# Kernel optimization log

Measured on AMD Instinct MI355X. Metric: run time of the kernel, lower is better.

The kernel has to match this reference:

```python
import jax, jax.numpy as jnp
import numpy as np

# --- static config (matches init_kwargs) ---
B, T, D, L = 32, 1024, 256, 10          # batch, signal length (2^L), feature dim, wavelet levels
V = T * D                                # |V| = 262144 graph nodes
ETA = 0.1
STEPS = 2                                # reaction_steps
INV_SQRT2 = 0.7071067811865476
BAND_SIZES = [T >> L] + [T >> l for l in range(L, 0, -1)]  # approx + details coarse->fine (n_levels+1 bands)


def haar_dwt(x):
    """x: (B,T,D) -> coeffs (B,T,D), layout [approx_L, d_L, d_{L-1}, ..., d_1]."""
    a = x
    details = []
    for _ in range(L):
        e, o = a[:, 0::2], a[:, 1::2]
        details.append((e - o) * INV_SQRT2)
        a = (e + o) * INV_SQRT2
    return jnp.concatenate([a] + details[::-1], axis=1)


def haar_idwt(c):
    """c: (B,T,D) in [approx, coarse..fine detail] layout -> signal (B,T,D)."""
    a = c[:, : T >> L]
    pos = T >> L
    for l in range(L, 0, -1):
        n = T >> l
        d = c[:, pos : pos + n]
        pos += n
        e = (a + d) * INV_SQRT2
        o = (a - d) * INV_SQRT2
        a = jnp.stack([e, o], axis=2).reshape(c.shape[0], 2 * n, D)  # interleave even/odd
    return a


def wavelet_linear(sig, W, b):
    """Per-band Linear(D->D): band i of the time axis uses W[i], b[i]."""
    outs = []
    pos = 0
    for i, n in enumerate(BAND_SIZES):
        seg = sig[:, pos : pos + n]  # (B, n, D)
        pos += n
        outs.append(jnp.einsum('btd,de->bte', seg, W[i]) + b[i])
    return jnp.concatenate(outs, axis=1)


def setup_inputs() -> dict:
    key = jax.random.key(0)
    k1, k2, k3, k4 = jax.random.split(key, 4)
    rho = jax.random.normal(k1, (B, V), dtype=jnp.float32)
    node_w = 0.5 + jax.random.uniform(k2, (V,), dtype=jnp.float32)            # graph node scaling (invertible)
    W = jax.random.normal(k3, (L + 1, D, D), dtype=jnp.float32) * 0.05        # per-band predictor weights
    b = jax.random.normal(k4, (L + 1, D), dtype=jnp.float32) * 0.01           # per-band bias
    return {"rho": rho, "node_w": node_w, "W": W, "b": b}


def reference(rho, node_w, W, b):
    for _ in range(STEPS):
        coeffs = (rho * node_w).reshape(B, T, D)          # graph.rho_to_coeffs
        coeffs_signal = haar_idwt(coeffs)                 # haar_idwt_1d
        predicted_signal = wavelet_linear(coeffs_signal, W, b)  # WaveletLinear predictor
        predicted_coeffs = haar_dwt(predicted_signal)     # haar_dwt_1d
        predicted_rho = predicted_coeffs.reshape(B, V) / node_w  # graph.coeffs_to_rho
        rho = rho - ETA * (rho - predicted_rho)           # PC error-reduction step
    return rho
```

## Files before the change

kernel.cpp:

```cpp
#include <hip/hip_runtime.h>
#include <hip/hip_bf16.h>

#define NB 32
#define NT 1024
#define ND 256
#define SP 264
#define ETA 0.1f
#define INVS 0.70710678118654752440f

typedef short bf16x8 __attribute__((ext_vector_type(8)));
typedef float f32x4  __attribute__((ext_vector_type(4)));

__device__ inline unsigned short f2bf(float f){
  __hip_bfloat16 h = __float2bfloat16(f);
  return *reinterpret_cast<unsigned short*>(&h);
}
__device__ inline float bf2f(unsigned short u){
  return __uint_as_float(((unsigned int)u) << 16);
}

template<int N>
__device__ inline void idwtT(float* a, const float* d){
#pragma unroll
  for (int i = N-1; i >= 0; --i){
    float av = a[i], dv = d[i];
    a[2*i]   = (av + dv) * INVS;
    a[2*i+1] = (av - dv) * INVS;
  }
}
template<int N>
__device__ inline void dwtT(float* a, float* d){
#pragma unroll
  for (int i = 0; i < N; ++i){
    float e = a[2*i], o = a[2*i+1];
    a[i] = (e + o) * INVS;
    d[i] = (e - o) * INVS;
  }
}
template<int N>
__device__ inline void dwt_sel2(float* x, int pj, float& pdet,
                                int j0, float& y0, int j1, float& y1){
#pragma unroll
  for (int i = 0; i < N; ++i){
    float e = x[2*i], o = x[2*i+1];
    float aa = (e + o) * INVS, dd = (e - o) * INVS;
    x[i] = aa;
    if (i == pj)    pdet = dd;
    if (N + i == j0) y0 = dd;
    if (N + i == j1) y1 = dd;
  }
}
template<int N>
__device__ inline void dwt_sel(float* x, int j, float& yj){
#pragma unroll
  for (int i = 0; i < N; ++i){
    float e = x[2*i], o = x[2*i+1];
    float aa = (e + o) * INVS, dd = (e - o) * INVS;
    x[i] = aa;
    if (N + i == j) yj = dd;
  }
}

__device__ inline void fine_rows(int j, int* fr){
  fr[0] = 64 + j;
#pragma unroll
  for (int i = 0; i < 2; ++i) fr[1+i] = 128 + 2*j + i;
#pragma unroll
  for (int i = 0; i < 4; ++i) fr[3+i] = 256 + 4*j + i;
#pragma unroll
  for (int i = 0; i < 8; ++i) fr[7+i] = 512 + 8*j + i;
}

__device__ inline void gemm_tile_lds(const unsigned short* ldsS,
                                     unsigned short* ldsY,
                                     const unsigned short* __restrict__ Wt,
                                     const float* __restrict__ bias,
                                     int band, int n0, int row16, int kg,
                                     int lo, int hi){
  const unsigned short* Wb = Wt + (size_t)band * 65536;
  bf16x8 breg[8][4];
#pragma unroll
  for (int kk = 0; kk < 8; ++kk)
#pragma unroll
    for (int ni = 0; ni < 4; ++ni)
      breg[kk][ni] = *(const bf16x8*)(Wb + (size_t)(n0 + 16*ni + row16)*256 + kk*32 + kg*8);
  float bv[4];
#pragma unroll
  for (int ni = 0; ni < 4; ++ni) bv[ni] = bias[band*256 + n0 + 16*ni + row16];

  f32x4 acc[2][4];
#pragma unroll
  for (int mi = 0; mi < 2; ++mi)
#pragma unroll
    for (int ni = 0; ni < 4; ++ni) acc[mi][ni] = (f32x4){0.f,0.f,0.f,0.f};

#pragma unroll
  for (int kk = 0; kk < 8; ++kk){
    bf16x8 a0 = *(const bf16x8*)&ldsS[row16*SP + kk*32 + kg*8];
    bf16x8 a1 = *(const bf16x8*)&ldsS[(16 + row16)*SP + kk*32 + kg*8];
#pragma unroll
    for (int ni = 0; ni < 4; ++ni){
      acc[0][ni] = __builtin_amdgcn_mfma_f32_16x16x32_bf16(a0, breg[kk][ni], acc[0][ni], 0,0,0);
      acc[1][ni] = __builtin_amdgcn_mfma_f32_16x16x32_bf16(a1, breg[kk][ni], acc[1][ni], 0,0,0);
    }
  }
#pragma unroll
  for (int ni = 0; ni < 4; ++ni)
#pragma unroll
    for (int mi = 0; mi < 2; ++mi)
#pragma unroll
      for (int jj = 0; jj < 4; ++jj){
        int trow = 16*mi + kg*4 + jj;
        if (trow >= lo && trow < hi)
          ldsY[trow*SP + n0 + 16*ni + row16] = f2bf(acc[mi][ni][jj] + bv[ni]);
      }
}

__global__ __launch_bounds__(256, 2) void k_big1(const float* __restrict__ rho,
                                                 const float* __restrict__ w,
                                                 const unsigned short* __restrict__ Wt,
                                                 const float* __restrict__ bias,
                                                 unsigned short* __restrict__ cf16,
                                                 float* __restrict__ st1){
  __shared__ __align__(16) unsigned short ldsS[32*SP];
  __shared__ __align__(16) unsigned short ldsY[32*SP];
  int bx = blockIdx.x;
  int b = bx & 31, p = bx >> 5;
  int col = threadIdx.x;
  int t0 = 32*p;
  size_t cb = (size_t)b*NT*ND;

  float cva[2][15];
  {
    int crow[7]; crow[0] = 0;
#pragma unroll
    for (int l = 6; l >= 1; --l) crow[7-l] = (64>>l) + ((2*p) >> l);
    float cpr[7];
#pragma unroll
    for (int i = 0; i < 7; ++i)
      cpr[i] = rho[cb + (size_t)crow[i]*ND + col] * w[(size_t)crow[i]*ND + col];
    float apre = cpr[0];
#pragma unroll
    for (int l = 6; l >= 2; --l){
      float s = (((2*p) >> (l-1)) & 1) ? -INVS : INVS;
      apre = apre*INVS + cpr[7-l]*s;
    }
#pragma unroll
    for (int jj = 0; jj < 2; ++jj){
      int j = 2*p + jj;
      float a = apre*INVS + cpr[6]*(jj ? -INVS : INVS);
      int fr[15]; fine_rows(j, fr);
      float f4, f3[2], f2a[4], f1[8];
      {
        float fv[15];
#pragma unroll
        for (int i = 0; i < 15; ++i){
          fv[i] = rho[cb + (size_t)fr[i]*ND + col] * w[(size_t)fr[i]*ND + col];
          cva[jj][i] = fv[i];
        }
        f4 = fv[0];
#pragma unroll
        for (int i = 0; i < 2; ++i) f3[i]  = fv[1+i];
#pragma unroll
        for (int i = 0; i < 4; ++i) f2a[i] = fv[3+i];
#pragma unroll
        for (int i = 0; i < 8; ++i) f1[i]  = fv[7+i];
      }
      float A[16]; A[0] = a;
      idwtT<1>(A, &f4); idwtT<2>(A, f3); idwtT<4>(A, f2a); idwtT<8>(A, f1);
#pragma unroll
      for (int i = 0; i < 16; ++i) ldsS[(16*jj + i)*SP + col] = f2bf(A[i]);
    }
  }
  __syncthreads();
  {
    int wv = threadIdx.x >> 6, lane = threadIdx.x & 63;
    int row16 = lane & 15, kg = lane >> 4, n0 = wv*64;
    if (p > 0){
      int band = 32 - __clz(t0);
      gemm_tile_lds(ldsS, ldsY, Wt, bias, band, n0, row16, kg, 0, 32);
    } else {
#pragma unroll
      for (int bd = 0; bd < 6; ++bd){
        int lo = (bd==0) ? 0 : (1<<(bd-1));
        int hi = (bd==0) ? 1 : (1<<bd);
        gemm_tile_lds(ldsS, ldsY, Wt, bias, bd, n0, row16, kg, lo, hi);
      }
    }
  }
  __syncthreads();
#pragma unroll
  for (int jj = 0; jj < 2; ++jj){
    int j = 2*p + jj;
    float x[16];
#pragma unroll
    for (int i = 0; i < 16; ++i) x[i] = bf2f(ldsY[(16*jj + i)*SP + col]);
    float d1[8], d2v[4], d3[2], d4v;
    dwtT<8>(x, d1); dwtT<4>(x, d2v); dwtT<2>(x, d3); dwtT<1>(x, &d4v);
    st1[((size_t)b*64 + j)*ND + col] = x[0];
    int fr[15]; fine_rows(j, fr);
    float det[15];
    det[0] = d4v;
#pragma unroll
    for (int i = 0; i < 2; ++i) det[1+i] = d3[i];
#pragma unroll
    for (int i = 0; i < 4; ++i) det[3+i] = d2v[i];
#pragma unroll
    for (int i = 0; i < 8; ++i) det[7+i] = d1[i];
#pragma unroll
    for (int i = 0; i < 15; ++i){
      float cv = cva[jj][i];
      cf16[cb + (size_t)fr[i]*ND + col] = f2bf(cv - ETA*(cv - det[i]));
    }
  }
}

__global__ __launch_bounds__(256, 2) void k_big2(const float* __restrict__ st1,
                                                 const float* __restrict__ rho,
                                                 const float* __restrict__ w,
                                                 const unsigned short* __restrict__ cf16,
                                                 const unsigned short* __restrict__ Wt,
                                                 const float* __restrict__ bias,
                                                 float* __restrict__ c,
                                                 float* __restrict__ st2){
  __shared__ __align__(16) unsigned short ldsS[32*SP];
  __shared__ __align__(16) unsigned short ldsY[32*SP];
  int bx = blockIdx.x;
  int b = bx & 31, p = bx >> 5;
  int col = threadIdx.x;
  int t0 = 32*p;
  size_t cb = (size_t)b*NT*ND;
  int j0 = 2*p, j1 = 2*p + 1;

  float cfa[2][15];
  {
    float x[64];
#pragma unroll
    for (int k = 0; k < 64; ++k) x[k] = st1[((size_t)b*64 + k)*ND + col];
    float pd[6], y0 = 0.f, y1 = 0.f;
    dwt_sel2<32>(x, j0>>1, pd[0], j0, y0, j1, y1);
    dwt_sel2<16>(x, j0>>2, pd[1], j0, y0, j1, y1);
    dwt_sel2< 8>(x, j0>>3, pd[2], j0, y0, j1, y1);
    dwt_sel2< 4>(x, j0>>4, pd[3], j0, y0, j1, y1);
    dwt_sel2< 2>(x, j0>>5, pd[4], j0, y0, j1, y1);
    dwt_sel2< 1>(x, j0>>6, pd[5], j0, y0, j1, y1);
    if (j0 == 0) y0 = x[0];

    float cpr[7];
    cpr[0] = rho[cb + col] * w[col];
#pragma unroll
    for (int l = 6; l >= 1; --l){
      int r = (64>>l) + (j0>>l);
      cpr[7-l] = rho[cb + (size_t)r*ND + col] * w[(size_t)r*ND + col];
    }
    {
      float cv = rho[cb + (size_t)j0*ND + col] * w[(size_t)j0*ND + col];
      c[cb + (size_t)j0*ND + col] = cv - ETA*(cv - y0);
      float cw = rho[cb + (size_t)j1*ND + col] * w[(size_t)j1*ND + col];
      c[cb + (size_t)j1*ND + col] = cw - ETA*(cw - y1);
    }
    float ncl[6];
#pragma unroll
    for (int l = 1; l <= 6; ++l){
      float cv = cpr[7-l];
      ncl[l-1] = cv - ETA*(cv - pd[l-1]);
    }
    float cvr = cpr[0];
    float apre = cvr - ETA*(cvr - x[0]);
#pragma unroll
    for (int l = 6; l >= 2; --l){
      float s = ((j0 >> (l-1)) & 1) ? -1.f : 1.f;
      apre = (apre + s*ncl[l-1]) * INVS;
    }
#pragma unroll
    for (int jj = 0; jj < 2; ++jj){
      int j = j0 + jj;
      float a = (apre + (jj ? -1.f : 1.f)*ncl[0]) * INVS;
      int fr[15]; fine_rows(j, fr);
      float f4, f3[2], f2a[4], f1[8];
      {
        float fv[15];
#pragma unroll
        for (int i = 0; i < 15; ++i){
          fv[i] = bf2f(cf16[cb + (size_t)fr[i]*ND + col]);
          cfa[jj][i] = fv[i];
        }
        f4 = fv[0];
#pragma unroll
        for (int i = 0; i < 2; ++i) f3[i]  = fv[1+i];
#pragma unroll
        for (int i = 0; i < 4; ++i) f2a[i] = fv[3+i];
#pragma unroll
        for (int i = 0; i < 8; ++i) f1[i]  = fv[7+i];
      }
      float A[16]; A[0] = a;
      idwtT<1>(A, &f4); idwtT<2>(A, f3); idwtT<4>(A, f2a); idwtT<8>(A, f1);
#pragma unroll
      for (int i = 0; i < 16; ++i) ldsS[(16*jj + i)*SP + col] = f2bf(A[i]);
    }
  }
  __syncthreads();
  {
    int wv = threadIdx.x >> 6, lane = threadIdx.x & 63;
    int row16 = lane & 15, kg = lane >> 4, n0 = wv*64;
    if (p > 0){
      int band = 32 - __clz(t0);
      gemm_tile_lds(ldsS, ldsY, Wt, bias, band, n0, row16, kg, 0, 32);
    } else {
#pragma unroll
      for (int bd = 0; bd < 6; ++bd){
        int lo = (bd==0) ? 0 : (1<<(bd-1));
        int hi = (bd==0) ? 1 : (1<<bd);
        gemm_tile_lds(ldsS, ldsY, Wt, bias, bd, n0, row16, kg, lo, hi);
      }
    }
  }
  __syncthreads();
#pragma unroll
  for (int jj = 0; jj < 2; ++jj){
    int j = j0 + jj;
    float x[16];
#pragma unroll
    for (int i = 0; i < 16; ++i) x[i] = bf2f(ldsY[(16*jj + i)*SP + col]);
    float d1[8], d2v[4], d3[2], d4v;
    dwtT<8>(x, d1); dwtT<4>(x, d2v); dwtT<2>(x, d3); dwtT<1>(x, &d4v);
    st2[((size_t)b*64 + j)*ND + col] = x[0];
    int fr[15]; fine_rows(j, fr);
    float det[15];
    det[0] = d4v;
#pragma unroll
    for (int i = 0; i < 2; ++i) det[1+i] = d3[i];
#pragma unroll
    for (int i = 0; i < 4; ++i) det[3+i] = d2v[i];
#pragma unroll
    for (int i = 0; i < 8; ++i) det[7+i] = d1[i];
#pragma unroll
    for (int i = 0; i < 15; ++i){
      float cv = cfa[jj][i];
      float ww = w[(size_t)fr[i]*ND + col];
      c[cb + (size_t)fr[i]*ND + col] = (cv - ETA*(cv - det[i])) / ww;
    }
  }
}

__global__ __launch_bounds__(256, 4) void k_fin2(const float* __restrict__ st2,
                                                 const float* __restrict__ w,
                                                 float* __restrict__ c){
  int b = blockIdx.y, j = blockIdx.x, d = threadIdx.x;
  size_t cb = (size_t)b*NT*ND;

  float x[64];
#pragma unroll
  for (int k = 0; k < 64; ++k) x[k] = st2[((size_t)b*64 + k)*ND + d];

  float cj = c[cb + (size_t)j*ND + d];
  float wj = w[(size_t)j*ND + d];

  float yj = 0.f;
  dwt_sel<32>(x, j, yj);
  dwt_sel<16>(x, j, yj);
  dwt_sel< 8>(x, j, yj);
  dwt_sel< 4>(x, j, yj);
  dwt_sel< 2>(x, j, yj);
  dwt_sel< 1>(x, j, yj);
  if (j == 0) yj = x[0];

  c[cb + (size_t)j*ND + d] = (cj - ETA*(cj - yj)) / wj;
}

__global__ __launch_bounds__(256) void k_wprep(const float* __restrict__ W,
                                               unsigned short* __restrict__ Wt){
  __shared__ float tbuf[32][33];
  int band = blockIdx.y;
  int tile = blockIdx.x;
  int td0 = (tile >> 3) * 32, te0 = (tile & 7) * 32;
  int tx = threadIdx.x & 31, ty = threadIdx.x >> 5;
#pragma unroll
  for (int i = 0; i < 4; ++i){
    tbuf[ty*4 + i][tx] = W[(size_t)band*65536 + (size_t)(td0 + ty*4 + i)*256 + te0 + tx];
  }
  __syncthreads();
#pragma unroll
  for (int i = 0; i < 4; ++i){
    Wt[(size_t)band*65536 + (size_t)(te0 + ty*4 + i)*256 + td0 + tx] = f2bf(tbuf[tx][ty*4 + i]);
  }
}

extern "C" void kernel_launch(void* const* d_in, const int* in_sizes, int n_in,
                              void* d_out, int out_size, void* d_ws, size_t ws_size,
                              hipStream_t stream){
  const float* rho  = (const float*)d_in[0];
  const float* w    = (const float*)d_in[1];
  const float* W    = (const float*)d_in[2];
  const float* bias = (const float*)d_in[3];

  float* c = (float*)d_out;
  unsigned short* Wt = (unsigned short*)d_ws;
  float* st1 = (float*)(Wt + (size_t)11 * 65536);
  float* st2 = st1 + (size_t)NB * 64 * ND;
  unsigned short* cf16 = (unsigned short*)(st2 + (size_t)NB * 64 * ND);

  k_wprep<<<dim3(64, 11), 256, 0, stream>>>(W, Wt);
  k_big1<<<NB*32, 256, 0, stream>>>(rho, w, Wt, bias, cf16, st1);
  k_big2<<<NB*32, 256, 0, stream>>>(st1, rho, w, cf16, Wt, bias, c, st2);
  k_fin2<<<dim3(64, NB), 256, 0, stream>>>(st2, w, c);
}
```

Baseline: 96.46 us.

## Share one LDS buffer, stream weights per k-step, raise occupancy to 4 blocks

Both fused kernels now use a single LDS tile instead of separate input and output tiles. GEMM results are kept in registers, and an extra barrier is added before they overwrite the input tile. Weight fragments are loaded from global memory inside the k loop rather than preloaded as 32 bf16x8 registers. Launch bounds go from 2 to 4 blocks per CU. The aim is to cut LDS and VGPR pressure so more waves stay resident and memory latency is hidden better, at the cost of an extra sync and weight loads interleaved with the MFMAs.

```diff
diff --git a/kernel.cpp b/kernel.cpp
--- a/kernel.cpp
+++ b/kernel.cpp
@@ -71,63 +71,81 @@
   for (int i = 0; i < 8; ++i) fr[7+i] = 512 + 8*j + i;
 }
 
-__device__ inline void gemm_tile_lds(const unsigned short* ldsS,
-                                     unsigned short* ldsY,
-                                     const unsigned short* __restrict__ Wt,
-                                     const float* __restrict__ bias,
-                                     int band, int n0, int row16, int kg,
-                                     int lo, int hi){
+__device__ inline void gemm_acc(const unsigned short* lds,
+                                const unsigned short* __restrict__ Wt,
+                                int band, int n0, int row16, int kg,
+                                f32x4 acc[2][4]){
   const unsigned short* Wb = Wt + (size_t)band * 65536;
-  bf16x8 breg[8][4];
-#pragma unroll
-  for (int kk = 0; kk < 8; ++kk)
-#pragma unroll
-    for (int ni = 0; ni < 4; ++ni)
-      breg[kk][ni] = *(const bf16x8*)(Wb + (size_t)(n0 + 16*ni + row16)*256 + kk*32 + kg*8);
-  float bv[4];
-#pragma unroll
-  for (int ni = 0; ni < 4; ++ni) bv[ni] = bias[band*256 + n0 + 16*ni + row16];
-
-  f32x4 acc[2][4];
 #pragma unroll
   for (int mi = 0; mi < 2; ++mi)
 #pragma unroll
     for (int ni = 0; ni < 4; ++ni) acc[mi][ni] = (f32x4){0.f,0.f,0.f,0.f};
-
 #pragma unroll
   for (int kk = 0; kk < 8; ++kk){
-    bf16x8 a0 = *(const bf16x8*)&ldsS[row16*SP + kk*32 + kg*8];
-    bf16x8 a1 = *(const bf16x8*)&ldsS[(16 + row16)*SP + kk*32 + kg*8];
+    bf16x8 a0 = *(const bf16x8*)&lds[row16*SP + kk*32 + kg*8];
+    bf16x8 a1 = *(const bf16x8*)&lds[(16 + row16)*SP + kk*32 + kg*8];
 #pragma unroll
     for (int ni = 0; ni < 4; ++ni){
-      acc[0][ni] = __builtin_amdgcn_mfma_f32_16x16x32_bf16(a0, breg[kk][ni], acc[0][ni], 0,0,0);
-      acc[1][ni] = __builtin_amdgcn_mfma_f32_16x16x32_bf16(a1, breg[kk][ni], acc[1][ni], 0,0,0);
-    }
-  }
-#pragma unroll
-  for (int ni = 0; ni < 4; ++ni)
+      bf16x8 bw = *(const bf16x8*)(Wb + (size_t)(n0 + 16*ni + row16)*256 + kk*32 + kg*8);
+      acc[0][ni] = __builtin_amdgcn_mfma_f32_16x16x32_bf16(a0, bw, acc[0][ni], 0,0,0);
+      acc[1][ni] = __builtin_amdgcn_mfma_f32_16x16x32_bf16(a1, bw, acc[1][ni], 0,0,0);
+    }
+  }
+}
+
+__device__ inline void gemm_phase(const unsigned short* lds,
+                                  const unsigned short* __restrict__ Wt,
+                                  const float* __restrict__ bias,
+                                  int p, int n0, int row16, int kg,
+                                  f32x4 fin[2][4]){
+  if (p > 0){
+    int band = 32 - __clz(32*p);
+    f32x4 acc[2][4];
+    gemm_acc(lds, Wt, band, n0, row16, kg, acc);
+    float bv[4];
+#pragma unroll
+    for (int ni = 0; ni < 4; ++ni) bv[ni] = bias[band*256 + n0 + 16*ni + row16];
 #pragma unroll
     for (int mi = 0; mi < 2; ++mi)
 #pragma unroll
-      for (int jj = 0; jj < 4; ++jj){
-        int trow = 16*mi + kg*4 + jj;
-        if (trow >= lo && trow < hi)
-          ldsY[trow*SP + n0 + 16*ni + row16] = f2bf(acc[mi][ni][jj] + bv[ni]);
-      }
-}
-
-__global__ __launch_bounds__(256, 2) void k_big1(const float* __restrict__ rho,
+      for (int ni = 0; ni < 4; ++ni)
+#pragma unroll
+        for (int jj = 0; jj < 4; ++jj)
+          fin[mi][ni][jj] = acc[mi][ni][jj] + bv[ni];
+  } else {
+#pragma unroll
+    for (int bd = 0; bd < 6; ++bd){
+      int lo = (bd==0) ? 0 : (1<<(bd-1));
+      int hi = (bd==0) ? 1 : (1<<bd);
+      f32x4 acc[2][4];
+      gemm_acc(lds, Wt, bd, n0, row16, kg, acc);
+      float bv[4];
+#pragma unroll
+      for (int ni = 0; ni < 4; ++ni) bv[ni] = bias[bd*256 + n0 + 16*ni + row16];
+#pragma unroll
+      for (int mi = 0; mi < 2; ++mi)
+#pragma unroll
+        for (int ni = 0; ni < 4; ++ni)
+#pragma unroll
+          for (int jj = 0; jj < 4; ++jj){
+            int trow = 16*mi + kg*4 + jj;
+            if (trow >= lo && trow < hi)
+              fin[mi][ni][jj] = acc[mi][ni][jj] + bv[ni];
+          }
+    }
+  }
+}
+
+__global__ __launch_bounds__(256, 4) void k_big1(const float* __restrict__ rho,
                                                  const float* __restrict__ w,
                                                  const unsigned short* __restrict__ Wt,
                                                  const float* __restrict__ bias,
                                                  unsigned short* __restrict__ cf16,
                                                  float* __restrict__ st1){
-  __shared__ __align__(16) unsigned short ldsS[32*SP];
-  __shared__ __align__(16) unsigned short ldsY[32*SP];
+  __shared__ __align__(16) unsigned short lds[32*SP];
   int bx = blockIdx.x;
   int b = bx & 31, p = bx >> 5;
   int col = threadIdx.x;
-  int t0 = 32*p;
   size_t cb = (size_t)b*NT*ND;
 
   float cva[2][15];
@@ -169,24 +187,29 @@
       float A[16]; A[0] = a;
       idwtT<1>(A, &f4); idwtT<2>(A, f3); idwtT<4>(A, f2a); idwtT<8>(A, f1);
 #pragma unroll
-      for (int i = 0; i < 16; ++i) ldsS[(16*jj + i)*SP + col] = f2bf(A[i]);
-    }
-  }
-  __syncthreads();
+      for (int i = 0; i < 16; ++i) lds[(16*jj + i)*SP + col] = f2bf(A[i]);
+    }
+  }
+  __syncthreads();
+  f32x4 fin[2][4];
   {
     int wv = threadIdx.x >> 6, lane = threadIdx.x & 63;
     int row16 = lane & 15, kg = lane >> 4, n0 = wv*64;
-    if (p > 0){
-      int band = 32 - __clz(t0);
-      gemm_tile_lds(ldsS, ldsY, Wt, bias, band, n0, row16, kg, 0, 32);
-    } else {
-#pragma unroll
-      for (int bd = 0; bd < 6; ++bd){
-        int lo = (bd==0) ? 0 : (1<<(bd-1));
-        int hi = (bd==0) ? 1 : (1<<bd);
-        gemm_tile_lds(ldsS, ldsY, Wt, bias, bd, n0, row16, kg, lo, hi);
-      }
-    }
+    gemm_phase(lds, Wt, bias, p, n0, row16, kg, fin);
+  }
+  __syncthreads();
+  {
+    int wv = threadIdx.x >> 6, lane = threadIdx.x & 63;
+    int row16 = lane & 15, kg = lane >> 4, n0 = wv*64;
+#pragma unroll
+    for (int ni = 0; ni < 4; ++ni)
+#pragma unroll
+      for (int mi = 0; mi < 2; ++mi)
+#pragma unroll
+        for (int jj = 0; jj < 4; ++jj){
+          int trow = 16*mi + kg*4 + jj;
+          lds[trow*SP + n0 + 16*ni + row16] = f2bf(fin[mi][ni][jj]);
+        }
   }
   __syncthreads();
 #pragma unroll
@@ -194,7 +217,7 @@
     int j = 2*p + jj;
     float x[16];
 #pragma unroll
-    for (int i = 0; i < 16; ++i) x[i] = bf2f(ldsY[(16*jj + i)*SP + col]);
+    for (int i = 0; i < 16; ++i) x[i] = bf2f(lds[(16*jj + i)*SP + col]);
     float d1[8], d2v[4], d3[2], d4v;
     dwtT<8>(x, d1); dwtT<4>(x, d2v); dwtT<2>(x, d3); dwtT<1>(x, &d4v);
     st1[((size_t)b*64 + j)*ND + col] = x[0];
@@ -215,7 +238,7 @@
   }
 }
 
-__global__ __launch_bounds__(256, 2) void k_big2(const float* __restrict__ st1,
+__global__ __launch_bounds__(256, 4) void k_big2(const float* __restrict__ st1,
                                                  const float* __restrict__ rho,
                                                  const float* __restrict__ w,
                                                  const unsigned short* __restrict__ cf16,
@@ -223,12 +246,10 @@
                                                  const float* __restrict__ bias,
                                                  float* __restrict__ c,
                                                  float* __restrict__ st2){
-  __shared__ __align__(16) unsigned short ldsS[32*SP];
-  __shared__ __align__(16) unsigned short ldsY[32*SP];
+  __shared__ __align__(16) unsigned short lds[32*SP];
   int bx = blockIdx.x;
   int b = bx & 31, p = bx >> 5;
   int col = threadIdx.x;
-  int t0 = 32*p;
   size_t cb = (size_t)b*NT*ND;
   int j0 = 2*p, j1 = 2*p + 1;
 
@@ -296,24 +317,29 @@
       float A[16]; A[0] = a;
       idwtT<1>(A, &f4); idwtT<2>(A, f3); idwtT<4>(A, f2a); idwtT<8>(A, f1);
 #pragma unroll
-      for (int i = 0; i < 16; ++i) ldsS[(16*jj + i)*SP + col] = f2bf(A[i]);
-    }
-  }
-  __syncthreads();
+      for (int i = 0; i < 16; ++i) lds[(16*jj + i)*SP + col] = f2bf(A[i]);
+    }
+  }
+  __syncthreads();
+  f32x4 fin[2][4];
   {
     int wv = threadIdx.x >> 6, lane = threadIdx.x & 63;
     int row16 = lane & 15, kg = lane >> 4, n0 = wv*64;
-    if (p > 0){
-      int band = 32 - __clz(t0);
-      gemm_tile_lds(ldsS, ldsY, Wt, bias, band, n0, row16, kg, 0, 32);
-    } else {
-#pragma unroll
-      for (int bd = 0; bd < 6; ++bd){
-        int lo = (bd==0) ? 0 : (1<<(bd-1));
-        int hi = (bd==0) ? 1 : (1<<bd);
-        gemm_tile_lds(ldsS, ldsY, Wt, bias, bd, n0, row16, kg, lo, hi);
-      }
-    }
+    gemm_phase(lds, Wt, bias, p, n0, row16, kg, fin);
+  }
+  __syncthreads();
+  {
+    int wv = threadIdx.x >> 6, lane = threadIdx.x & 63;
+    int row16 = lane & 15, kg = lane >> 4, n0 = wv*64;
+#pragma unroll
+    for (int ni = 0; ni < 4; ++ni)
+#pragma unroll
+      for (int mi = 0; mi < 2; ++mi)
+#pragma unroll
+        for (int jj = 0; jj < 4; ++jj){
+          int trow = 16*mi + kg*4 + jj;
+          lds[trow*SP + n0 + 16*ni + row16] = f2bf(fin[mi][ni][jj]);
+        }
   }
   __syncthreads();
 #pragma unroll
@@ -321,7 +347,7 @@
     int j = j0 + jj;
     float x[16];
 #pragma unroll
-    for (int i = 0; i < 16; ++i) x[i] = bf2f(ldsY[(16*jj + i)*SP + col]);
+    for (int i = 0; i < 16; ++i) x[i] = bf2f(lds[(16*jj + i)*SP + col]);
     float d1[8], d2v[4], d3[2], d4v;
     dwtT<8>(x, d1); dwtT<4>(x, d2v); dwtT<2>(x, d3); dwtT<1>(x, &d4v);
     st2[((size_t)b*64 + j)*ND + col] = x[0];
```

Measured after the change: 118.1 us. +22.5%, slower.

## Halve per-block tile to 16 time rows, doubling grid and cutting LDS

Applied to the files above, without the earlier changes.

Each block of the two main kernels now handles one 16-row group (one j index) instead of two, so the grid doubles to 2048 blocks and the shared-memory tiles shrink by half. The GEMM now streams weight fragments from global memory inside the k loop instead of preloading 32 registers' worth, and uses a single 16-row MFMA tile. The band mapping is reworked so j=1 uses band 5 and j=0 spans bands 0-4. The aim is higher occupancy and lower register pressure, at the cost of reading each weight tile twice as often and recomputing the coarse prefix per block.

```diff
diff --git a/kernel.cpp b/kernel.cpp
--- a/kernel.cpp
+++ b/kernel.cpp
@@ -38,16 +38,14 @@
   }
 }
 template<int N>
-__device__ inline void dwt_sel2(float* x, int pj, float& pdet,
-                                int j0, float& y0, int j1, float& y1){
+__device__ inline void dwt_selp(float* x, int pj, float& pdet, int j, float& yj){
 #pragma unroll
   for (int i = 0; i < N; ++i){
     float e = x[2*i], o = x[2*i+1];
     float aa = (e + o) * INVS, dd = (e - o) * INVS;
     x[i] = aa;
-    if (i == pj)    pdet = dd;
-    if (N + i == j0) y0 = dd;
-    if (N + i == j1) y1 = dd;
+    if (i == pj)     pdet = dd;
+    if (N + i == j)  yj = dd;
   }
 }
 template<int N>
@@ -71,49 +69,57 @@
   for (int i = 0; i < 8; ++i) fr[7+i] = 512 + 8*j + i;
 }
 
-__device__ inline void gemm_tile_lds(const unsigned short* ldsS,
-                                     unsigned short* ldsY,
-                                     const unsigned short* __restrict__ Wt,
-                                     const float* __restrict__ bias,
-                                     int band, int n0, int row16, int kg,
-                                     int lo, int hi){
+__device__ inline void gemm_acc16(const unsigned short* lds,
+                                  const unsigned short* __restrict__ Wt,
+                                  int band, int n0, int row16, int kg,
+                                  f32x4 acc[4]){
   const unsigned short* Wb = Wt + (size_t)band * 65536;
-  bf16x8 breg[8][4];
-#pragma unroll
-  for (int kk = 0; kk < 8; ++kk)
-#pragma unroll
-    for (int ni = 0; ni < 4; ++ni)
-      breg[kk][ni] = *(const bf16x8*)(Wb + (size_t)(n0 + 16*ni + row16)*256 + kk*32 + kg*8);
-  float bv[4];
-#pragma unroll
-  for (int ni = 0; ni < 4; ++ni) bv[ni] = bias[band*256 + n0 + 16*ni + row16];
-
-  f32x4 acc[2][4];
-#pragma unroll
-  for (int mi = 0; mi < 2; ++mi)
-#pragma unroll
-    for (int ni = 0; ni < 4; ++ni) acc[mi][ni] = (f32x4){0.f,0.f,0.f,0.f};
-
+#pragma unroll
+  for (int ni = 0; ni < 4; ++ni) acc[ni] = (f32x4){0.f,0.f,0.f,0.f};
 #pragma unroll
   for (int kk = 0; kk < 8; ++kk){
-    bf16x8 a0 = *(const bf16x8*)&ldsS[row16*SP + kk*32 + kg*8];
-    bf16x8 a1 = *(const bf16x8*)&ldsS[(16 + row16)*SP + kk*32 + kg*8];
+    bf16x8 a0 = *(const bf16x8*)&lds[row16*SP + kk*32 + kg*8];
 #pragma unroll
     for (int ni = 0; ni < 4; ++ni){
-      acc[0][ni] = __builtin_amdgcn_mfma_f32_16x16x32_bf16(a0, breg[kk][ni], acc[0][ni], 0,0,0);
-      acc[1][ni] = __builtin_amdgcn_mfma_f32_16x16x32_bf16(a1, breg[kk][ni], acc[1][ni], 0,0,0);
-    }
-  }
-#pragma unroll
-  for (int ni = 0; ni < 4; ++ni)
-#pragma unroll
-    for (int mi = 0; mi < 2; ++mi)
-#pragma unroll
-      for (int jj = 0; jj < 4; ++jj){
-        int trow = 16*mi + kg*4 + jj;
-        if (trow >= lo && trow < hi)
-          ldsY[trow*SP + n0 + 16*ni + row16] = f2bf(acc[mi][ni][jj] + bv[ni]);
-      }
+      bf16x8 bw = *(const bf16x8*)(Wb + (size_t)(n0 + 16*ni + row16)*256 + kk*32 + kg*8);
+      acc[ni] = __builtin_amdgcn_mfma_f32_16x16x32_bf16(a0, bw, acc[ni], 0,0,0);
+    }
+  }
+}
+
+__device__ inline void gemm_phase16(const unsigned short* ldsS,
+                                    const unsigned short* __restrict__ Wt,
+                                    const float* __restrict__ bias,
+                                    int j, int n0, int row16, int kg,
+                                    f32x4 fin[4]){
+  if (j >= 1){
+    int band = (j == 1) ? 5 : (32 - __clz(16*j));
+    f32x4 acc[4];
+    gemm_acc16(ldsS, Wt, band, n0, row16, kg, acc);
+#pragma unroll
+    for (int ni = 0; ni < 4; ++ni){
+      float bv = bias[band*256 + n0 + 16*ni + row16];
+#pragma unroll
+      for (int jj = 0; jj < 4; ++jj) fin[ni][jj] = acc[ni][jj] + bv;
+    }
+  } else {
+#pragma unroll
+    for (int bd = 0; bd < 5; ++bd){
+      int lo = (bd==0) ? 0 : (1<<(bd-1));
+      int hi = (bd==0) ? 1 : (1<<bd);
+      f32x4 acc[4];
+      gemm_acc16(ldsS, Wt, bd, n0, row16, kg, acc);
+#pragma unroll
+      for (int ni = 0; ni < 4; ++ni){
+        float bv = bias[bd*256 + n0 + 16*ni + row16];
+#pragma unroll
+        for (int jj = 0; jj < 4; ++jj){
+          int trow = kg*4 + jj;
+          if (trow >= lo && trow < hi) fin[ni][jj] = acc[ni][jj] + bv;
+        }
+      }
+    }
+  }
 }
 
 __global__ __launch_bounds__(256, 2) void k_big1(const float* __restrict__ rho,
@@ -122,79 +128,69 @@
                                                  const float* __restrict__ bias,
                                                  unsigned short* __restrict__ cf16,
                                                  float* __restrict__ st1){
-  __shared__ __align__(16) unsigned short ldsS[32*SP];
-  __shared__ __align__(16) unsigned short ldsY[32*SP];
+  __shared__ __align__(16) unsigned short ldsS[16*SP];
+  __shared__ __align__(16) unsigned short ldsY[16*SP];
   int bx = blockIdx.x;
-  int b = bx & 31, p = bx >> 5;
+  int b = bx & 31, j = bx >> 5;
   int col = threadIdx.x;
-  int t0 = 32*p;
   size_t cb = (size_t)b*NT*ND;
 
-  float cva[2][15];
+  float cva[15];
   {
     int crow[7]; crow[0] = 0;
 #pragma unroll
-    for (int l = 6; l >= 1; --l) crow[7-l] = (64>>l) + ((2*p) >> l);
+    for (int l = 6; l >= 1; --l) crow[7-l] = (64>>l) + (j>>l);
     float cpr[7];
 #pragma unroll
     for (int i = 0; i < 7; ++i)
       cpr[i] = rho[cb + (size_t)crow[i]*ND + col] * w[(size_t)crow[i]*ND + col];
-    float apre = cpr[0];
-#pragma unroll
-    for (int l = 6; l >= 2; --l){
-      float s = (((2*p) >> (l-1)) & 1) ? -INVS : INVS;
-      apre = apre*INVS + cpr[7-l]*s;
-    }
-#pragma unroll
-    for (int jj = 0; jj < 2; ++jj){
-      int j = 2*p + jj;
-      float a = apre*INVS + cpr[6]*(jj ? -INVS : INVS);
-      int fr[15]; fine_rows(j, fr);
-      float f4, f3[2], f2a[4], f1[8];
-      {
-        float fv[15];
-#pragma unroll
-        for (int i = 0; i < 15; ++i){
-          fv[i] = rho[cb + (size_t)fr[i]*ND + col] * w[(size_t)fr[i]*ND + col];
-          cva[jj][i] = fv[i];
-        }
-        f4 = fv[0];
-#pragma unroll
-        for (int i = 0; i < 2; ++i) f3[i]  = fv[1+i];
-#pragma unroll
-        for (int i = 0; i < 4; ++i) f2a[i] = fv[3+i];
-#pragma unroll
-        for (int i = 0; i < 8; ++i) f1[i]  = fv[7+i];
-      }
-      float A[16]; A[0] = a;
-      idwtT<1>(A, &f4); idwtT<2>(A, f3); idwtT<4>(A, f2a); idwtT<8>(A, f1);
-#pragma unroll
-      for (int i = 0; i < 16; ++i) ldsS[(16*jj + i)*SP + col] = f2bf(A[i]);
-    }
+    float a = cpr[0];
+#pragma unroll
+    for (int l = 6; l >= 1; --l){
+      float s = ((j >> (l-1)) & 1) ? -INVS : INVS;
+      a = a*INVS + cpr[7-l]*s;
+    }
+    int fr[15]; fine_rows(j, fr);
+    float f4, f3[2], f2a[4], f1[8];
+    {
+      float fv[15];
+#pragma unroll
+      for (int i = 0; i < 15; ++i){
+        fv[i] = rho[cb + (size_t)fr[i]*ND + col] * w[(size_t)fr[i]*ND + col];
+        cva[i] = fv[i];
+      }
+      f4 = fv[0];
+#pragma unroll
+      for (int i = 0; i < 2; ++i) f3[i]  = fv[1+i];
+#pragma unroll
+      for (int i = 0; i < 4; ++i) f2a[i] = fv[3+i];
+#pragma unroll
+      for (int i = 0; i < 8; ++i) f1[i]  = fv[7+i];
+    }
+    float A[16]; A[0] = a;
+    idwtT<1>(A, &f4); idwtT<2>(A, f3); idwtT<4>(A, f2a); idwtT<8>(A, f1);
+#pragma unroll
+    for (int i = 0; i < 16; ++i) ldsS[i*SP + col] = f2bf(A[i]);
   }
   __syncthreads();
   {
     int wv = threadIdx.x >> 6, lane = threadIdx.x & 63;
     int row16 = lane & 15, kg = lane >> 4, n0 = wv*64;
-    if (p > 0){
-      int band = 32 - __clz(t0);
-      gemm_tile_lds(ldsS, ldsY, Wt, bias, band, n0, row16, kg, 0, 32);
-    } else {
-#pragma unroll
-      for (int bd = 0; bd < 6; ++bd){
-        int lo = (bd==0) ? 0 : (1<<(bd-1));
-        int hi = (bd==0) ? 1 : (1<<bd);
-        gemm_tile_lds(ldsS, ldsY, Wt, bias, bd, n0, row16, kg, lo, hi);
-      }
-    }
-  }
-  __syncthreads();
-#pragma unroll
-  for (int jj = 0; jj < 2; ++jj){
-    int j = 2*p + jj;
+    f32x4 fin[4];
+    gemm_phase16(ldsS, Wt, bias, j, n0, row16, kg, fin);
+#pragma unroll
+    for (int ni = 0; ni < 4; ++ni)
+#pragma unroll
+      for (int jj = 0; jj < 4; ++jj){
+        int trow = kg*4 + jj;
+        ldsY[trow*SP + n0 + 16*ni + row16] = f2bf(fin[ni][jj]);
+      }
+  }
+  __syncthreads();
+  {
     float x[16];
 #pragma unroll
-    for (int i = 0; i < 16; ++i) x[i] = bf2f(ldsY[(16*jj + i)*SP + col]);
+    for (int i = 0; i < 16; ++i) x[i] = bf2f(ldsY[i*SP + col]);
     float d1[8], d2v[4], d3[2], d4v;
     dwtT<8>(x, d1); dwtT<4>(x, d2v); dwtT<2>(x, d3); dwtT<1>(x, &d4v);
     st1[((size_t)b*64 + j)*ND + col] = x[0];
@@ -209,7 +205,7 @@
     for (int i = 0; i < 8; ++i) det[7+i] = d1[i];
 #pragma unroll
     for (int i = 0; i < 15; ++i){
-      float cv = cva[jj][i];
+      float cv = cva[i];
       cf16[cb + (size_t)fr[i]*ND + col] = f2bf(cv - ETA*(cv - det[i]));
     }
   }
@@ -223,41 +219,37 @@
                                                  const float* __restrict__ bias,
                                                  float* __restrict__ c,
                                                  float* __restrict__ st2){
-  __shared__ __align__(16) unsigned short ldsS[32*SP];
-  __shared__ __align__(16) unsigned short ldsY[32*SP];
+  __shared__ __align__(16) unsigned short ldsS[16*SP];
+  __shared__ __align__(16) unsigned short ldsY[16*SP];
   int bx = blockIdx.x;
-  int b = bx & 31, p = bx >> 5;
+  int b = bx & 31, j = bx >> 5;
   int col = threadIdx.x;
-  int t0 = 32*p;
   size_t cb = (size_t)b*NT*ND;
-  int j0 = 2*p, j1 = 2*p + 1;
-
-  float cfa[2][15];
+
+  float cfa[15];
   {
     float x[64];
 #pragma unroll
     for (int k = 0; k < 64; ++k) x[k] = st1[((size_t)b*64 + k)*ND + col];
-    float pd[6], y0 = 0.f, y1 = 0.f;
-    dwt_sel2<32>(x, j0>>1, pd[0], j0, y0, j1, y1);
-    dwt_sel2<16>(x, j0>>2, pd[1], j0, y0, j1, y1);
-    dwt_sel2< 8>(x, j0>>3, pd[2], j0, y0, j1, y1);
-    dwt_sel2< 4>(x, j0>>4, pd[3], j0, y0, j1, y1);
-    dwt_sel2< 2>(x, j0>>5, pd[4], j0, y0, j1, y1);
-    dwt_sel2< 1>(x, j0>>6, pd[5], j0, y0, j1, y1);
-    if (j0 == 0) y0 = x[0];
+    float pd[6], yj = 0.f;
+    dwt_selp<32>(x, j>>1, pd[0], j, yj);
+    dwt_selp<16>(x, j>>2, pd[1], j, yj);
+    dwt_selp< 8>(x, j>>3, pd[2], j, yj);
+    dwt_selp< 4>(x, j>>4, pd[3], j, yj);
+    dwt_selp< 2>(x, j>>5, pd[4], j, yj);
+    dwt_selp< 1>(x, j>>6, pd[5], j, yj);
+    if (j == 0) yj = x[0];
 
     float cpr[7];
     cpr[0] = rho[cb + col] * w[col];
 #pragma unroll
     for (int l = 6; l >= 1; --l){
-      int r = (64>>l) + (j0>>l);
+      int r = (64>>l) + (j>>l);
       cpr[7-l] = rho[cb + (size_t)r*ND + col] * w[(size_t)r*ND + col];
     }
     {
-      float cv = rho[cb + (size_t)j0*ND + col] * w[(size_t)j0*ND + col];
-      c[cb + (size_t)j0*ND + col] = cv - ETA*(cv - y0);
-      float cw = rho[cb + (size_t)j1*ND + col] * w[(size_t)j1*ND + col];
-      c[cb + (size_t)j1*ND + col] = cw - ETA*(cw - y1);
+      float cv = rho[cb + (size_t)j*ND + col] * w[(size_t)j*ND + col];
+      c[cb + (size_t)j*ND + col] = cv - ETA*(cv - yj);
     }
     float ncl[6];
 #pragma unroll
@@ -266,62 +258,53 @@
       ncl[l-1] = cv - ETA*(cv - pd[l-1]);
     }
     float cvr = cpr[0];
-    float apre = cvr - ETA*(cvr - x[0]);
-#pragma unroll
-    for (int l = 6; l >= 2; --l){
-      float s = ((j0 >> (l-1)) & 1) ? -1.f : 1.f;
-      apre = (apre + s*ncl[l-1]) * INVS;
-    }
-#pragma unroll
-    for (int jj = 0; jj < 2; ++jj){
-      int j = j0 + jj;
-      float a = (apre + (jj ? -1.f : 1.f)*ncl[0]) * INVS;
-      int fr[15]; fine_rows(j, fr);
-      float f4, f3[2], f2a[4], f1[8];
-      {
-        float fv[15];
-#pragma unroll
-        for (int i = 0; i < 15; ++i){
-          fv[i] = bf2f(cf16[cb + (size_t)fr[i]*ND + col]);
-          cfa[jj][i] = fv[i];
-        }
-        f4 = fv[0];
-#pragma unroll
-        for (int i = 0; i < 2; ++i) f3[i]  = fv[1+i];
-#pragma unroll
-        for (int i = 0; i < 4; ++i) f2a[i] = fv[3+i];
-#pragma unroll
-        for (int i = 0; i < 8; ++i) f1[i]  = fv[7+i];
-      }
-      float A[16]; A[0] = a;
-      idwtT<1>(A, &f4); idwtT<2>(A, f3); idwtT<4>(A, f2a); idwtT<8>(A, f1);
-#pragma unroll
-      for (int i = 0; i < 16; ++i) ldsS[(16*jj + i)*SP + col] = f2bf(A[i]);
-    }
+    float a = cvr - ETA*(cvr - x[0]);
+#pragma unroll
+    for (int l = 6; l >= 1; --l){
+      float s = ((j >> (l-1)) & 1) ? -1.f : 1.f;
+      a = (a + s*ncl[l-1]) * INVS;
+    }
+    int fr[15]; fine_rows(j, fr);
+    float f4, f3[2], f2a[4], f1[8];
+    {
+      float fv[15];
+#pragma unroll
+      for (int i = 0; i < 15; ++i){
+        fv[i] = bf2f(cf16[cb + (size_t)fr[i]*ND + col]);
+        cfa[i] = fv[i];
+      }
+      f4 = fv[0];
+#pragma unroll
+      for (int i = 0; i < 2; ++i) f3[i]  = fv[1+i];
+#pragma unroll
+      for (int i = 0; i < 4; ++i) f2a[i] = fv[3+i];
+#pragma unroll
+      for (int i = 0; i < 8; ++i) f1[i]  = fv[7+i];
+    }
+    float A[16]; A[0] = a;
+    idwtT<1>(A, &f4); idwtT<2>(A, f3); idwtT<4>(A, f2a); idwtT<8>(A, f1);
+#pragma unroll
+    for (int i = 0; i < 16; ++i) ldsS[i*SP + col] = f2bf(A[i]);
   }
   __syncthreads();
   {
     int wv = threadIdx.x >> 6, lane = threadIdx.x & 63;
     int row16 = lane & 15, kg = lane >> 4, n0 = wv*64;
-    if (p > 0){
-      int band = 32 - __clz(t0);
-      gemm_tile_lds(ldsS, ldsY, Wt, bias, band, n0, row16, kg, 0, 32);
-    } else {
-#pragma unroll
-      for (int bd = 0; bd < 6; ++bd){
-        int lo = (bd==0) ? 0 : (1<<(bd-1));
-        int hi = (bd==0) ? 1 : (1<<bd);
-        gemm_tile_lds(ldsS, ldsY, Wt, bias, bd, n0, row16, kg, lo, hi);
-      }
-    }
-  }
-  __syncthreads();
-#pragma unroll
-  for (int jj = 0; jj < 2; ++jj){
-    int j = j0 + jj;
+    f32x4 fin[4];
+    gemm_phase16(ldsS, Wt, bias, j, n0, row16, kg, fin);
+#pragma unroll
+    for (int ni = 0; ni < 4; ++ni)
+#pragma unroll
+      for (int jj = 0; jj < 4; ++jj){
+        int trow = kg*4 + jj;
+        ldsY[trow*SP + n0 + 16*ni + row16] = f2bf(fin[ni][jj]);
+      }
+  }
+  __syncthreads();
+  {
     float x[16];
 #pragma unroll
-    for (int i = 0; i < 16; ++i) x[i] = bf2f(ldsY[(16*jj + i)*SP + col]);
+    for (int i = 0; i < 16; ++i) x[i] = bf2f(ldsY[i*SP + col]);
     float d1[8], d2v[4], d3[2], d4v;
     dwtT<8>(x, d1); dwtT<4>(x, d2v); dwtT<2>(x, d3); dwtT<1>(x, &d4v);
     st2[((size_t)b*64 + j)*ND + col] = x[0];
@@ -336,7 +319,7 @@
     for (int i = 0; i < 8; ++i) det[7+i] = d1[i];
 #pragma unroll
     for (int i = 0; i < 15; ++i){
-      float cv = cfa[jj][i];
+      float cv = cfa[i];
       float ww = w[(size_t)fr[i]*ND + col];
       c[cb + (size_t)fr[i]*ND + col] = (cv - ETA*(cv - det[i])) / ww;
     }
@@ -401,7 +384,7 @@
   unsigned short* cf16 = (unsigned short*)(st2 + (size_t)NB * 64 * ND);
 
   k_wprep<<<dim3(64, 11), 256, 0, stream>>>(W, Wt);
-  k_big1<<<NB*32, 256, 0, stream>>>(rho, w, Wt, bias, cf16, st1);
-  k_big2<<<NB*32, 256, 0, stream>>>(st1, rho, w, cf16, Wt, bias, c, st2);
+  k_big1<<<NB*64, 256, 0, stream>>>(rho, w, Wt, bias, cf16, st1);
+  k_big2<<<NB*64, 256, 0, stream>>>(st1, rho, w, cf16, Wt, bias, c, st2);
   k_fin2<<<dim3(64, NB), 256, 0, stream>>>(st2, w, c);
 }
```

After: 122.6 us. 1.27x slower.
